# Kernel optimization log

Measured on AMD Instinct MI355X. Metric: run time of the kernel, lower is better.

The kernel has to match this reference:

```python
import jax, jax.numpy as jnp
import numpy as np

N = 768
C = 256  # in_features == out_features (required by Linear(in_features+3, 1))

def _leaky(x):
    return jnp.where(x >= 0, x, 0.2 * x)

def setup_inputs() -> dict:
    key = jax.random.key(0)
    ks = jax.random.split(key, 10)
    features = jax.random.normal(ks[0], (N, C), dtype=jnp.float32)
    coordinates = jax.random.normal(ks[1], (N, 3), dtype=jnp.float32)
    adj = jax.random.uniform(ks[2], (N, N), dtype=jnp.float32)  # unused by forward, kept for signature fidelity
    # Learned params
    FC = jax.random.normal(ks[3], (C, C), dtype=jnp.float32) * (1.414 / jnp.sqrt(C))
    # Conv1d(2,1,kernel=1): weight [out=1, in=2, k=1] -> 2 scalars + bias
    fc_w = jax.random.normal(ks[4], (2,), dtype=jnp.float32) * 0.5
    fc_b = jax.random.normal(ks[5], (1,), dtype=jnp.float32) * 0.1
    sc_w = jax.random.normal(ks[6], (2,), dtype=jnp.float32) * 0.5
    sc_b = jax.random.normal(ks[7], (1,), dtype=jnp.float32) * 0.1
    # Linear(C+3, 1)
    lin_w = jax.random.normal(ks[8], (C + 3,), dtype=jnp.float32) * (1.0 / jnp.sqrt(C + 3))
    lin_b = jax.random.normal(ks[9], (1,), dtype=jnp.float32) * 0.1
    return {"features": features, "coordinates": coordinates, "adj": adj,
            "FC": FC, "fc_w": fc_w, "fc_b": fc_b, "sc_w": sc_w, "sc_b": sc_b,
            "lin_w": lin_w, "lin_b": lin_b}

def reference(features, coordinates, adj, FC, fc_w, fc_b, sc_w, sc_b, lin_w, lin_b):
    n = features.shape[0]
    f_input = features @ FC  # [N, C]
    # torch's repeat(1,N).view + repeat(N,1) builds pairs (i, j); the 1x1 Conv1d over
    # the 2 stacked channels is exactly w0*x_i + w1*x_j + b, then LeakyReLU(0.2).
    f_map = _leaky(fc_w[0] * f_input[:, None, :] + fc_w[1] * f_input[None, :, :] + fc_b[0])  # [N,N,C]
    s_map = _leaky(sc_w[0] * coordinates[:, None, :] + sc_w[1] * coordinates[None, :, :] + sc_b[0])  # [N,N,3]
    # Linear(C+3, 1) on cat([f_map, s_map], -1), then LeakyReLU -> [N, N]
    scores = _leaky(jnp.einsum('ijc,c->ij', f_map, lin_w[:f_input.shape[1]])
                    + jnp.einsum('ijk,k->ij', s_map, lin_w[f_input.shape[1]:])
                    + lin_b[0])
    attention = jax.nn.softmax(scores, axis=1)  # row softmax (dim=1)
    h_prime = attention @ f_input  # [N, C]
    return jax.nn.elu(h_prime)  # concat=True path
```

## Files before the change

kernel.cpp:

```cpp
#include <hip/hip_runtime.h>
#include <math.h>

#define NN 768
#define CC 256
#define TI 3
#define JC 256
#define NJC 3

__device__ __forceinline__ float leaky(float x) { return x >= 0.0f ? x : 0.2f * x; }

__device__ __forceinline__ float waveMax(float v) {
    #pragma unroll
    for (int o = 32; o > 0; o >>= 1) v = fmaxf(v, __shfl_xor(v, o, 64));
    return v;
}
__device__ __forceinline__ float waveSum(float v) {
    #pragma unroll
    for (int o = 32; o > 0; o >>= 1) v += __shfl_xor(v, o, 64);
    return v;
}

__global__ __launch_bounds__(768) void k_prep(
    const float* __restrict__ features,
    const float* __restrict__ FC,
    const float* __restrict__ fc_w,
    const float* __restrict__ fc_b,
    const float* __restrict__ lin_w,
    float* __restrict__ f,
    float* __restrict__ g,
    float* __restrict__ D0,
    float* __restrict__ D1,
    float4* __restrict__ ut4)
{
    __shared__ float sA[TI * CC];
    __shared__ float sF[TI * CC];
    __shared__ float sredD[12], sredW[12];

    const int t  = threadIdx.x;
    const int r  = t >> 8;
    const int c  = t & 255;
    const int i0 = blockIdx.x * TI;

    sA[r * CC + c] = features[(i0 + r) * CC + c];
    __syncthreads();

    float a = 0.f;
    const float* fcp = FC + c;
    const float* ap  = sA + r * CC;
    #pragma unroll 8
    for (int k = 0; k < CC; ++k)
        a = fmaf(ap[k], fcp[k * CC], a);

    const float w1 = fc_w[1], b = fc_b[0];
    f[(i0 + r) * CC + c] = a;
    g[c * NN + i0 + r]   = fmaf(w1, a, b);
    sF[r * CC + c] = a;

    const float lw = lin_w[c];
    float dv = waveSum(lw * a);
    float wv = waveSum(lw);
    const int wid = t >> 6;
    if ((t & 63) == 0) { sredD[wid] = dv; sredW[wid] = wv; }
    __syncthreads();
    if (t < TI) {
        float D = sredD[t*4] + sredD[t*4+1] + sredD[t*4+2] + sredD[t*4+3];
        float W = sredW[t*4] + sredW[t*4+1] + sredW[t*4+2] + sredW[t*4+3];
        D0[i0 + t] = fc_w[0] * D;
        D1[i0 + t] = fmaf(w1, D, b * W);
    }
    if (t < CC) {
        const float w0 = fc_w[0];
        ut4[blockIdx.x * CC + t] = make_float4(w0 * sF[t],
                                               w0 * sF[CC + t],
                                               w0 * sF[2*CC + t],
                                               0.4f * lin_w[t]);
    }
}

__global__ __launch_bounds__(256) void k_attn(
    const float* __restrict__ f,
    const float* __restrict__ g,
    const float4* __restrict__ ut4,
    const float* __restrict__ D0,
    const float* __restrict__ D1,
    const float* __restrict__ coords,
    const float* __restrict__ sc_w,
    const float* __restrict__ sc_b,
    const float* __restrict__ lin_w,
    const float* __restrict__ lin_b,
    float* __restrict__ hp,
    float* __restrict__ Mp,
    float* __restrict__ Lp)
{
    __shared__ float4 pp[JC];
    __shared__ float  hpart[4][TI][CC];
    __shared__ float4 sredm4[4];
    __shared__ float4 sreds4[4];

    const int t    = threadIdx.x;
    const int it   = blockIdx.x & 255;
    const int jc   = blockIdx.x >> 8;
    const int i0   = it * TI;
    const int jb   = jc * JC;
    const int j    = jb + t;
    const int w    = t >> 6;
    const int lane = t & 63;

    float a0 = 0.f, a1 = 0.f, a2 = 0.f;
    const float4* up = ut4 + (size_t)it * CC;
    const float*  gp = g + j;
    #pragma unroll 8
    for (int c = 0; c < CC; ++c) {
        float  gj = gp[c * NN];
        float4 u  = up[c];
        a0 = fmaf(u.w, fabsf(u.x + gj), a0);
        a1 = fmaf(u.w, fabsf(u.y + gj), a1);
        a2 = fmaf(u.w, fabsf(u.z + gj), a2);
    }

    const float sw0 = sc_w[0], sw1 = sc_w[1], sb = sc_b[0], lb = lin_b[0];
    const float lw30 = lin_w[CC], lw31 = lin_w[CC+1], lw32 = lin_w[CC+2];
    const float cj0 = fmaf(sw1, coords[j*3+0], sb);
    const float cj1 = fmaf(sw1, coords[j*3+1], sb);
    const float cj2 = fmaf(sw1, coords[j*3+2], sb);
    const float d1  = D1[j];
    float accs[3] = {a0, a1, a2};
    float scv[3];
    #pragma unroll
    for (int rr = 0; rr < TI; ++rr) {
        const int i = i0 + rr;
        float sd = lw30 * leaky(fmaf(sw0, coords[i*3+0], cj0))
                 + lw31 * leaky(fmaf(sw0, coords[i*3+1], cj1))
                 + lw32 * leaky(fmaf(sw0, coords[i*3+2], cj2));
        scv[rr] = leaky(accs[rr] + sd + 0.6f * (D0[i] + d1) + lb);
    }

    {
        float v0 = waveMax(scv[0]);
        float v1 = waveMax(scv[1]);
        float v2 = waveMax(scv[2]);
        if (lane == 0) sredm4[w] = make_float4(v0, v1, v2, 0.f);
    }
    __syncthreads();
    float m[TI];
    {
        float4 x0 = sredm4[0], x1 = sredm4[1], x2 = sredm4[2], x3 = sredm4[3];
        m[0] = fmaxf(fmaxf(x0.x, x1.x), fmaxf(x2.x, x3.x));
        m[1] = fmaxf(fmaxf(x0.y, x1.y), fmaxf(x2.y, x3.y));
        m[2] = fmaxf(fmaxf(x0.z, x1.z), fmaxf(x2.z, x3.z));
    }
    float e0 = __expf(scv[0] - m[0]);
    float e1 = __expf(scv[1] - m[1]);
    float e2 = __expf(scv[2] - m[2]);
    pp[t] = make_float4(e0, e1, e2, 0.f);
    {
        float v0 = waveSum(e0);
        float v1 = waveSum(e1);
        float v2 = waveSum(e2);
        if (lane == 0) sreds4[w] = make_float4(v0, v1, v2, 0.f);
    }
    __syncthreads();
    if (t < TI) {
        float4 s0 = sreds4[0], s1 = sreds4[1], s2 = sreds4[2], s3 = sreds4[3];
        float l = (t == 0) ? (s0.x + s1.x + s2.x + s3.x)
                : (t == 1) ? (s0.y + s1.y + s2.y + s3.y)
                           : (s0.z + s1.z + s2.z + s3.z);
        float mm = (t == 0) ? m[0] : (t == 1) ? m[1] : m[2];
        Mp[(i0 + t) * NJC + jc] = mm;
        Lp[(i0 + t) * NJC + jc] = l;
    }

    float4 h0 = make_float4(0.f,0.f,0.f,0.f);
    float4 h1 = h0, h2 = h0;
    const float4* f4 = (const float4*)f;
    const int jsl = w * 64;
    #pragma unroll 4
    for (int jx = 0; jx < 64; ++jx) {
        const int jl = jsl + jx;
        float4 fv = f4[(size_t)(jb + jl) * 64 + lane];
        float4 e  = pp[jl];
        h0.x = fmaf(e.x, fv.x, h0.x); h0.y = fmaf(e.x, fv.y, h0.y);
        h0.z = fmaf(e.x, fv.z, h0.z); h0.w = fmaf(e.x, fv.w, h0.w);
        h1.x = fmaf(e.y, fv.x, h1.x); h1.y = fmaf(e.y, fv.y, h1.y);
        h1.z = fmaf(e.y, fv.z, h1.z); h1.w = fmaf(e.y, fv.w, h1.w);
        h2.x = fmaf(e.z, fv.x, h2.x); h2.y = fmaf(e.z, fv.y, h2.y);
        h2.z = fmaf(e.z, fv.z, h2.z); h2.w = fmaf(e.z, fv.w, h2.w);
    }
    *(float4*)&hpart[w][0][4*lane] = h0;
    *(float4*)&hpart[w][1][4*lane] = h1;
    *(float4*)&hpart[w][2][4*lane] = h2;
    __syncthreads();

    #pragma unroll
    for (int r = 0; r < TI; ++r) {
        float h = hpart[0][r][t] + hpart[1][r][t] + hpart[2][r][t] + hpart[3][r][t];
        hp[((size_t)jc * NN + i0 + r) * CC + t] = h;
    }
}

__global__ __launch_bounds__(256) void k_comb(
    const float* __restrict__ hp,
    const float* __restrict__ Mp,
    const float* __restrict__ Lp,
    float* __restrict__ out)
{
    const int t = threadIdx.x;
    const int i = blockIdx.x;

    float m0 = Mp[i*NJC+0], m1 = Mp[i*NJC+1], m2 = Mp[i*NJC+2];
    float M  = fmaxf(fmaxf(m0, m1), m2);
    float w0 = __expf(m0 - M), w1 = __expf(m1 - M), w2 = __expf(m2 - M);
    float den = w0*Lp[i*NJC+0] + w1*Lp[i*NJC+1] + w2*Lp[i*NJC+2];
    float inv = 1.0f / den;

    float num = w0 * hp[((size_t)0*NN + i)*CC + t]
              + w1 * hp[((size_t)1*NN + i)*CC + t]
              + w2 * hp[((size_t)2*NN + i)*CC + t];
    float v = num * inv;
    out[i*CC + t] = (v > 0.f) ? v : (__expf(v) - 1.0f);
}

extern "C" void kernel_launch(void* const* d_in, const int* in_sizes, int n_in,
                              void* d_out, int out_size, void* d_ws, size_t ws_size,
                              hipStream_t stream) {
    const float* features = (const float*)d_in[0];
    const float* coords   = (const float*)d_in[1];
    const float* FC       = (const float*)d_in[3];
    const float* fc_w     = (const float*)d_in[4];
    const float* fc_b     = (const float*)d_in[5];
    const float* sc_w     = (const float*)d_in[6];
    const float* sc_b     = (const float*)d_in[7];
    const float* lin_w    = (const float*)d_in[8];
    const float* lin_b    = (const float*)d_in[9];
    float* out = (float*)d_out;

    float* f  = (float*)d_ws;
    float* g  = f  + NN*CC;
    float* D0 = g  + CC*NN;
    float* D1 = D0 + NN;
    float* Mp = D1 + NN;
    float* Lp = Mp + NN*NJC;
    float* hp = Lp + NN*NJC;
    float4* ut4;
    {
        size_t off = (size_t)((char*)(hp + (size_t)NJC*NN*CC) - (char*)d_ws);
        off = (off + 15) & ~(size_t)15;
        ut4 = (float4*)((char*)d_ws + off);
    }

    k_prep<<<NN/TI, 768, 0, stream>>>(features, FC, fc_w, fc_b, lin_w, f, g, D0, D1, ut4);
    k_attn<<<(NN/TI)*NJC, 256, 0, stream>>>(f, g, ut4, D0, D1, coords, sc_w, sc_b,
                                            lin_w, lin_b, hp, Mp, Lp);
    k_comb<<<NN, 256, 0, stream>>>(hp, Mp, Lp, out);
}
```

Measured before the change: 116.9 us.

## Split score channel loop across waves with float4 j-vectorized loads and LDS reduction

The score accumulation in the attention kernel is re-partitioned. Previously each thread summed over all 256 channels for a single j. Now each wave covers a 64-channel slice, and each lane handles 4 consecutive j values through float4 loads of g, with the four wave partial sums combined through a new shared-memory buffer and a barrier. This cuts the serial loop length and uses wider loads, at the cost of extra LDS (about 12KB more), an added sync, and fewer blocks able to reside per CU.

```diff
diff --git a/kernel.cpp b/kernel.cpp
--- a/kernel.cpp
+++ b/kernel.cpp
@@ -92,6 +92,7 @@
     float* __restrict__ Mp,
     float* __restrict__ Lp)
 {
+    __shared__ float  spart[4][TI][JC];
     __shared__ float4 pp[JC];
     __shared__ float  hpart[4][TI][CC];
     __shared__ float4 sredm4[4];
@@ -106,17 +107,43 @@
     const int w    = t >> 6;
     const int lane = t & 63;
 
-    float a0 = 0.f, a1 = 0.f, a2 = 0.f;
-    const float4* up = ut4 + (size_t)it * CC;
-    const float*  gp = g + j;
+    float4 a0 = make_float4(0.f,0.f,0.f,0.f);
+    float4 a1 = a0, a2 = a0;
+    const float4* gq = (const float4*)g + (size_t)(w << 6) * (NN/4) + (jb >> 2) + lane;
+    const float4* up = ut4 + (size_t)it * CC + (w << 6);
     #pragma unroll 8
-    for (int c = 0; c < CC; ++c) {
-        float  gj = gp[c * NN];
-        float4 u  = up[c];
-        a0 = fmaf(u.w, fabsf(u.x + gj), a0);
-        a1 = fmaf(u.w, fabsf(u.y + gj), a1);
-        a2 = fmaf(u.w, fabsf(u.z + gj), a2);
-    }
+    for (int cc = 0; cc < 64; ++cc) {
+        float4 gv = gq[cc * (NN/4)];
+        float4 u  = up[cc];
+        a0.x = fmaf(u.w, fabsf(u.x + gv.x), a0.x);
+        a0.y = fmaf(u.w, fabsf(u.x + gv.y), a0.y);
+        a0.z = fmaf(u.w, fabsf(u.x + gv.z), a0.z);
+        a0.w = fmaf(u.w, fabsf(u.x + gv.w), a0.w);
+        a1.x = fmaf(u.w, fabsf(u.y + gv.x), a1.x);
+        a1.y = fmaf(u.w, fabsf(u.y + gv.y), a1.y);
+        a1.z = fmaf(u.w, fabsf(u.y + gv.z), a1.z);
+        a1.w = fmaf(u.w, fabsf(u.y + gv.w), a1.w);
+        a2.x = fmaf(u.w, fabsf(u.z + gv.x), a2.x);
+        a2.y = fmaf(u.w, fabsf(u.z + gv.y), a2.y);
+        a2.z = fmaf(u.w, fabsf(u.z + gv.z), a2.z);
+        a2.w = fmaf(u.w, fabsf(u.z + gv.w), a2.w);
+    }
+    {
+        const int jl4 = 4 * lane;
+        spart[w][0][jl4+0] = a0.x; spart[w][0][jl4+1] = a0.y;
+        spart[w][0][jl4+2] = a0.z; spart[w][0][jl4+3] = a0.w;
+        spart[w][1][jl4+0] = a1.x; spart[w][1][jl4+1] = a1.y;
+        spart[w][1][jl4+2] = a1.z; spart[w][1][jl4+3] = a1.w;
+        spart[w][2][jl4+0] = a2.x; spart[w][2][jl4+1] = a2.y;
+        spart[w][2][jl4+2] = a2.z; spart[w][2][jl4+3] = a2.w;
+    }
+    __syncthreads();
+
+    float accs[3];
+    #pragma unroll
+    for (int rr = 0; rr < TI; ++rr)
+        accs[rr] = spart[0][rr][t] + spart[1][rr][t]
+                 + spart[2][rr][t] + spart[3][rr][t];
 
     const float sw0 = sc_w[0], sw1 = sc_w[1], sb = sc_b[0], lb = lin_b[0];
     const float lw30 = lin_w[CC], lw31 = lin_w[CC+1], lw32 = lin_w[CC+2];
@@ -124,7 +151,6 @@
     const float cj1 = fmaf(sw1, coords[j*3+1], sb);
     const float cj2 = fmaf(sw1, coords[j*3+2], sb);
     const float d1  = D1[j];
-    float accs[3] = {a0, a1, a2};
     float scv[3];
     #pragma unroll
     for (int rr = 0; rr < TI; ++rr) {
```

After: 115.9 us. No clear change (-0.9%).

## Tile attention kernel over 12 rows with channel-split score reduction

Applied to the files above, without the earlier changes.

The attention kernel now processes 12 query rows per block instead of 3, with 192 blocks instead of 768. In the score phase each wave takes a quarter of the channels for 4 columns via float4 loads of g, and the partial sums are reduced through shared memory. Each loaded g and f value is reused across 12 rows, cutting global traffic per FLOP. The cost is much higher register use (12 float4 accumulators in two phases), more shared memory and fewer blocks, which may lower occupancy and leave parts of the GPU idle.

```diff
diff --git a/kernel.cpp b/kernel.cpp
--- a/kernel.cpp
+++ b/kernel.cpp
@@ -4,8 +4,10 @@
 #define NN 768
 #define CC 256
 #define TI 3
-#define JC 256
+#define RT 12
+#define JCC 256
 #define NJC 3
+#define PSTR 20
 
 __device__ __forceinline__ float leaky(float x) { return x >= 0.0f ? x : 0.2f * x; }
 
@@ -18,6 +20,19 @@
     #pragma unroll
     for (int o = 32; o > 0; o >>= 1) v += __shfl_xor(v, o, 64);
     return v;
+}
+
+__device__ __forceinline__ void acc_row(float4& a, float ur, float w4, const float4& gv) {
+    a.x = fmaf(w4, fabsf(ur + gv.x), a.x);
+    a.y = fmaf(w4, fabsf(ur + gv.y), a.y);
+    a.z = fmaf(w4, fabsf(ur + gv.z), a.z);
+    a.w = fmaf(w4, fabsf(ur + gv.w), a.w);
+}
+__device__ __forceinline__ void fma4(float4& h, float e, const float4& fv) {
+    h.x = fmaf(e, fv.x, h.x);
+    h.y = fmaf(e, fv.y, h.y);
+    h.z = fmaf(e, fv.z, h.z);
+    h.w = fmaf(e, fv.w, h.w);
 }
 
 __global__ __launch_bounds__(768) void k_prep(
@@ -92,109 +107,122 @@
     float* __restrict__ Mp,
     float* __restrict__ Lp)
 {
-    __shared__ float4 pp[JC];
-    __shared__ float  hpart[4][TI][CC];
-    __shared__ float4 sredm4[4];
-    __shared__ float4 sreds4[4];
+    __shared__ float4 su4[4][CC];
+    __shared__ float  sred[4][RT][CC];
+    __shared__ float  pe[JCC][PSTR];
+    __shared__ float  sredm[4][RT];
+    __shared__ float  sreds[4][RT];
 
     const int t    = threadIdx.x;
-    const int it   = blockIdx.x & 255;
-    const int jc   = blockIdx.x >> 8;
-    const int i0   = it * TI;
-    const int jb   = jc * JC;
-    const int j    = jb + t;
+    const int it   = blockIdx.x & 63;
+    const int jc   = blockIdx.x >> 6;
+    const int i0   = it * RT;
+    const int jb   = jc * JCC;
     const int w    = t >> 6;
     const int lane = t & 63;
 
-    float a0 = 0.f, a1 = 0.f, a2 = 0.f;
-    const float4* up = ut4 + (size_t)it * CC;
-    const float*  gp = g + j;
-    #pragma unroll 8
-    for (int c = 0; c < CC; ++c) {
-        float  gj = gp[c * NN];
-        float4 u  = up[c];
-        a0 = fmaf(u.w, fabsf(u.x + gj), a0);
-        a1 = fmaf(u.w, fabsf(u.y + gj), a1);
-        a2 = fmaf(u.w, fabsf(u.z + gj), a2);
-    }
-
+    #pragma unroll
+    for (int q = 0; q < 4; ++q)
+        su4[q][t] = ut4[(size_t)(it * 4 + q) * CC + t];
+    __syncthreads();
+
+    float4 acc[RT];
+    #pragma unroll
+    for (int r = 0; r < RT; ++r) acc[r] = make_float4(0.f, 0.f, 0.f, 0.f);
+    const float4* gq = (const float4*)g + (size_t)(w << 6) * (NN/4) + (jb >> 2) + lane;
+    #pragma unroll 4
+    for (int cc = 0; cc < 64; ++cc) {
+        float4 gv = gq[(size_t)cc * (NN/4)];
+        const int c = (w << 6) + cc;
+        #pragma unroll
+        for (int q = 0; q < 4; ++q) {
+            float4 u = su4[q][c];
+            acc_row(acc[3*q+0], u.x, u.w, gv);
+            acc_row(acc[3*q+1], u.y, u.w, gv);
+            acc_row(acc[3*q+2], u.z, u.w, gv);
+        }
+    }
+    #pragma unroll
+    for (int r = 0; r < RT; ++r)
+        *(float4*)&sred[w][r][4*lane] = acc[r];
+    __syncthreads();
+
+    const int j = jb + t;
     const float sw0 = sc_w[0], sw1 = sc_w[1], sb = sc_b[0], lb = lin_b[0];
     const float lw30 = lin_w[CC], lw31 = lin_w[CC+1], lw32 = lin_w[CC+2];
     const float cj0 = fmaf(sw1, coords[j*3+0], sb);
     const float cj1 = fmaf(sw1, coords[j*3+1], sb);
     const float cj2 = fmaf(sw1, coords[j*3+2], sb);
     const float d1  = D1[j];
-    float accs[3] = {a0, a1, a2};
-    float scv[3];
-    #pragma unroll
-    for (int rr = 0; rr < TI; ++rr) {
-        const int i = i0 + rr;
+    float scv[RT];
+    #pragma unroll
+    for (int r = 0; r < RT; ++r) {
+        const int i = i0 + r;
+        float a = sred[0][r][t] + sred[1][r][t] + sred[2][r][t] + sred[3][r][t];
         float sd = lw30 * leaky(fmaf(sw0, coords[i*3+0], cj0))
                  + lw31 * leaky(fmaf(sw0, coords[i*3+1], cj1))
                  + lw32 * leaky(fmaf(sw0, coords[i*3+2], cj2));
-        scv[rr] = leaky(accs[rr] + sd + 0.6f * (D0[i] + d1) + lb);
-    }
-
-    {
-        float v0 = waveMax(scv[0]);
-        float v1 = waveMax(scv[1]);
-        float v2 = waveMax(scv[2]);
-        if (lane == 0) sredm4[w] = make_float4(v0, v1, v2, 0.f);
-    }
-    __syncthreads();
-    float m[TI];
-    {
-        float4 x0 = sredm4[0], x1 = sredm4[1], x2 = sredm4[2], x3 = sredm4[3];
-        m[0] = fmaxf(fmaxf(x0.x, x1.x), fmaxf(x2.x, x3.x));
-        m[1] = fmaxf(fmaxf(x0.y, x1.y), fmaxf(x2.y, x3.y));
-        m[2] = fmaxf(fmaxf(x0.z, x1.z), fmaxf(x2.z, x3.z));
-    }
-    float e0 = __expf(scv[0] - m[0]);
-    float e1 = __expf(scv[1] - m[1]);
-    float e2 = __expf(scv[2] - m[2]);
-    pp[t] = make_float4(e0, e1, e2, 0.f);
-    {
-        float v0 = waveSum(e0);
-        float v1 = waveSum(e1);
-        float v2 = waveSum(e2);
-        if (lane == 0) sreds4[w] = make_float4(v0, v1, v2, 0.f);
-    }
-    __syncthreads();
-    if (t < TI) {
-        float4 s0 = sreds4[0], s1 = sreds4[1], s2 = sreds4[2], s3 = sreds4[3];
-        float l = (t == 0) ? (s0.x + s1.x + s2.x + s3.x)
-                : (t == 1) ? (s0.y + s1.y + s2.y + s3.y)
-                           : (s0.z + s1.z + s2.z + s3.z);
-        float mm = (t == 0) ? m[0] : (t == 1) ? m[1] : m[2];
+        scv[r] = leaky(a + sd + 0.6f * (D0[i] + d1) + lb);
+    }
+
+    #pragma unroll
+    for (int r = 0; r < RT; ++r) {
+        float v = waveMax(scv[r]);
+        if (lane == 0) sredm[w][r] = v;
+    }
+    __syncthreads();
+    float m[RT];
+    #pragma unroll
+    for (int r = 0; r < RT; ++r)
+        m[r] = fmaxf(fmaxf(sredm[0][r], sredm[1][r]),
+                     fmaxf(sredm[2][r], sredm[3][r]));
+    float e[RT];
+    #pragma unroll
+    for (int r = 0; r < RT; ++r) {
+        e[r] = __expf(scv[r] - m[r]);
+        pe[t][r] = e[r];
+    }
+    #pragma unroll
+    for (int r = 0; r < RT; ++r) {
+        float v = waveSum(e[r]);
+        if (lane == 0) sreds[w][r] = v;
+    }
+    __syncthreads();
+    if (t < RT) {
+        float l  = sreds[0][t] + sreds[1][t] + sreds[2][t] + sreds[3][t];
+        float mm = fmaxf(fmaxf(sredm[0][t], sredm[1][t]),
+                         fmaxf(sredm[2][t], sredm[3][t]));
         Mp[(i0 + t) * NJC + jc] = mm;
         Lp[(i0 + t) * NJC + jc] = l;
     }
 
-    float4 h0 = make_float4(0.f,0.f,0.f,0.f);
-    float4 h1 = h0, h2 = h0;
+    float4 h[RT];
+    #pragma unroll
+    for (int r = 0; r < RT; ++r) h[r] = make_float4(0.f, 0.f, 0.f, 0.f);
     const float4* f4 = (const float4*)f;
     const int jsl = w * 64;
-    #pragma unroll 4
+    #pragma unroll 2
     for (int jx = 0; jx < 64; ++jx) {
         const int jl = jsl + jx;
         float4 fv = f4[(size_t)(jb + jl) * 64 + lane];
-        float4 e  = pp[jl];
-        h0.x = fmaf(e.x, fv.x, h0.x); h0.y = fmaf(e.x, fv.y, h0.y);
-        h0.z = fmaf(e.x, fv.z, h0.z); h0.w = fmaf(e.x, fv.w, h0.w);
-        h1.x = fmaf(e.y, fv.x, h1.x); h1.y = fmaf(e.y, fv.y, h1.y);
-        h1.z = fmaf(e.y, fv.z, h1.z); h1.w = fmaf(e.y, fv.w, h1.w);
-        h2.x = fmaf(e.z, fv.x, h2.x); h2.y = fmaf(e.z, fv.y, h2.y);
-        h2.z = fmaf(e.z, fv.z, h2.z); h2.w = fmaf(e.z, fv.w, h2.w);
-    }
-    *(float4*)&hpart[w][0][4*lane] = h0;
-    *(float4*)&hpart[w][1][4*lane] = h1;
-    *(float4*)&hpart[w][2][4*lane] = h2;
-    __syncthreads();
-
-    #pragma unroll
-    for (int r = 0; r < TI; ++r) {
-        float h = hpart[0][r][t] + hpart[1][r][t] + hpart[2][r][t] + hpart[3][r][t];
-        hp[((size_t)jc * NN + i0 + r) * CC + t] = h;
+        const float4* pe4 = (const float4*)&pe[jl][0];
+        float4 e0 = pe4[0], e1 = pe4[1], e2 = pe4[2];
+        fma4(h[0],  e0.x, fv); fma4(h[1],  e0.y, fv);
+        fma4(h[2],  e0.z, fv); fma4(h[3],  e0.w, fv);
+        fma4(h[4],  e1.x, fv); fma4(h[5],  e1.y, fv);
+        fma4(h[6],  e1.z, fv); fma4(h[7],  e1.w, fv);
+        fma4(h[8],  e2.x, fv); fma4(h[9],  e2.y, fv);
+        fma4(h[10], e2.z, fv); fma4(h[11], e2.w, fv);
+    }
+    #pragma unroll
+    for (int r = 0; r < RT; ++r)
+        *(float4*)&sred[w][r][4*lane] = h[r];
+    __syncthreads();
+
+    #pragma unroll
+    for (int r = 0; r < RT; ++r) {
+        float hh = sred[0][r][t] + sred[1][r][t] + sred[2][r][t] + sred[3][r][t];
+        hp[((size_t)jc * NN + i0 + r) * CC + t] = hh;
     }
 }
 
@@ -249,7 +277,7 @@
     }
 
     k_prep<<<NN/TI, 768, 0, stream>>>(features, FC, fc_w, fc_b, lin_w, f, g, D0, D1, ut4);
-    k_attn<<<(NN/TI)*NJC, 256, 0, stream>>>(f, g, ut4, D0, D1, coords, sc_w, sc_b,
+    k_attn<<<(NN/RT)*NJC, 256, 0, stream>>>(f, g, ut4, D0, D1, coords, sc_w, sc_b,
                                             lin_w, lin_b, hp, Mp, Lp);
     k_comb<<<NN, 256, 0, stream>>>(hp, Mp, Lp, out);
 }
```

Measured after the change: 128.8 us. 10.2% more time.
